# Optimization experiments

Measured on AMD Instinct MI355X. Metric: run time of the kernel, lower is better.

The kernel has to match this reference:

```python
import jax, jax.numpy as jnp
from jax import lax
import numpy as np

B, C, N, MAX_OUT = 8, 16, 2048, 100


def setup_inputs() -> dict:
    key = jax.random.key(0)
    kc, kw, ks = jax.random.split(key, 3)
    # well-formed xyxy boxes: centers in [0,1000), sizes in [1,101)
    ctr = jax.random.uniform(kc, (B, N, 2), jnp.float32) * 1000.0
    wh = jax.random.uniform(kw, (B, N, 2), jnp.float32) * 100.0 + 1.0
    boxes = jnp.concatenate([ctr - wh * 0.5, ctr + wh * 0.5], axis=-1)  # [B,N,4]
    scores = jax.random.uniform(ks, (B, C, N), jnp.float32)  # [B,C,N]
    return {
        "boxes": boxes,
        "scores": scores,
        "max_output_boxes_per_class": MAX_OUT,
        "iou_threshold": jnp.array([0.5], jnp.float32),
        "score_threshold": jnp.array([0.5], jnp.float32),
    }


def _pairwise_iou(bx):
    # bx: [N,4] xyxy -> [N,N] IoU (matches torchvision.ops.box_iou)
    x1, y1, x2, y2 = bx[:, 0], bx[:, 1], bx[:, 2], bx[:, 3]
    area = (x2 - x1) * (y2 - y1)
    iw = jnp.clip(jnp.minimum(x2[:, None], x2[None, :]) - jnp.maximum(x1[:, None], x1[None, :]), 0.0)
    ih = jnp.clip(jnp.minimum(y2[:, None], y2[None, :]) - jnp.maximum(y1[:, None], y1[None, :]), 0.0)
    inter = iw * ih
    return inter / (area[:, None] + area[None, :] - inter)


def _nms_selected(boxes, scores, iou_threshold, score_threshold, max_out):
    # boxes [B,N,4], scores [B,C,N]
    b, c, n = scores.shape
    iou = jax.vmap(_pairwise_iou)(boxes)  # [B,N,N], shared across classes
    iou_t = iou_threshold.reshape(())
    score_t = score_threshold.reshape(())

    def one_class(iou_b, cls_scores):
        order = jnp.argsort(-cls_scores)          # descending score order [N]
        valid = cls_scores[order] > score_t       # strict >, as in the torch code

        def step(suppressed, inp):
            ok, bi = inp
            kept = ok & (~suppressed[bi])
            # greedy suppression: a kept box removes all boxes with IoU > thr
            suppressed = suppressed | (kept & (iou_b[bi] > iou_t))
            return suppressed, kept

        _, keep = lax.scan(step, jnp.zeros((n,), bool), (valid, order))
        rank = jnp.cumsum(keep.astype(jnp.int32)) - 1
        sel = keep & (rank < max_out)
        pos = jnp.where(sel, rank, max_out)  # overflow/non-selected -> dropped slot
        buf = jnp.full((max_out + 1,), -1, jnp.int32).at[pos].set(
            jnp.where(sel, order.astype(jnp.int32), -1))
        return buf[:max_out]  # box indices in score order, -1 padded

    per_bc = jax.vmap(lambda iou_b, sb: jax.vmap(lambda s: one_class(iou_b, s))(sb))(iou, scores)  # [B,C,max_out]
    b_idx = jnp.broadcast_to(jnp.arange(b, dtype=jnp.int32)[:, None, None], per_bc.shape)
    c_idx = jnp.broadcast_to(jnp.arange(c, dtype=jnp.int32)[None, :, None], per_bc.shape)
    rows = jnp.stack([b_idx, c_idx, per_bc], axis=-1).reshape(-1, 3)  # [B*C*max_out, 3]
    # invalid (padded) rows are all -1
    return jnp.where(rows[:, 2:3] >= 0, rows, -1)


def reference(boxes, scores, max_output_boxes_per_class, iou_threshold, score_threshold):
    return _nms_selected(boxes, scores, iou_threshold, score_threshold,
                         int(max_output_boxes_per_class))
```

## Files before the change

kernel.cpp:

```cpp
#include <hip/hip_runtime.h>
#include <stdint.h>


#define NBOX 2048
#define THREADS 1024
#define CHUNK 128
#define MAXKEEP 256

typedef unsigned long long u64;

__device__ __forceinline__ u64 ce_x(u64 v, int s, bool up, int lane) {
  u64 p = __shfl_xor(v, s, 64);
  bool lower = ((lane & s) == 0);
  u64 mx = v > p ? v : p;
  u64 mn = v > p ? p : v;
  return (up == lower) ? mx : mn;
}

__global__ __launch_bounds__(THREADS) void nms_kernel(
    const float* __restrict__ boxes,
    const float* __restrict__ scores,
    const int* __restrict__ maxOutPtr,
    const float* __restrict__ iouThrPtr,
    const float* __restrict__ scoreThrPtr,
    int* __restrict__ out,
    int B, int C, int slots)
{
  __shared__ u64 skeys[NBOX];
  __shared__ float sx1[NBOX], sy1[NBOX], sx2[NBOX], sy2[NBOX], sar[NBOX];
  __shared__ unsigned colmask[CHUNK][4];
  __shared__ unsigned char suppPre[CHUNK];
  __shared__ int keptPos[MAXKEEP];
  __shared__ int Vsh, cntSh;

  const int tid  = threadIdx.x;
  const int lane = tid & 63;
  const int w    = tid >> 6;
  const int bc = blockIdx.x;
  const int b = bc / C, c = bc % C;
  const float iouT   = iouThrPtr[0];
  const float scoreT = scoreThrPtr[0];
  int mOut = maxOutPtr[0];
  if (mOut > slots) mOut = slots;
  if (mOut > MAXKEEP) mOut = MAXKEEP;
  if (mOut < 0) mOut = 0;

  const float* cls = scores + ((size_t)b * C + c) * NBOX;
  if (tid == 0) { Vsh = 0; cntSh = 0; }

  const int j0 = w * 128 + lane;
  const int j1 = j0 + 64;
  float s0 = cls[j0], s1 = cls[j1];
  unsigned u0 = __float_as_uint(s0); u0 = (u0 & 0x80000000u) ? ~u0 : (u0 | 0x80000000u);
  unsigned u1 = __float_as_uint(s1); u1 = (u1 & 0x80000000u) ? ~u1 : (u1 | 0x80000000u);
  u64 e0 = ((u64)u0 << 32) | (0xFFFFFFFFu - (unsigned)j0);
  u64 e1 = ((u64)u1 << 32) | (0xFFFFFFFFu - (unsigned)j1);
  int pop = __popcll(__ballot(s0 > scoreT)) + __popcll(__ballot(s1 > scoreT));

  #pragma unroll
  for (int k = 2; k <= 64; k <<= 1) {
    #pragma unroll
    for (int s = k >> 1; s >= 1; s >>= 1) {
      bool up0 = ((lane & k) == 0);
      bool up1 = (((64 + lane) & k) == 0);
      e0 = ce_x(e0, s, up0, lane);
      e1 = ce_x(e1, s, up1, lane);
    }
  }
  {
    bool up = ((w & 1) == 0);
    u64 mx = e0 > e1 ? e0 : e1, mn = e0 > e1 ? e1 : e0;
    e0 = up ? mx : mn; e1 = up ? mn : mx;
    #pragma unroll
    for (int s = 32; s >= 1; s >>= 1) {
      e0 = ce_x(e0, s, up, lane);
      e1 = ce_x(e1, s, up, lane);
    }
  }
  skeys[j0] = e0; skeys[j1] = e1;
  __syncthreads();
  if (lane == 0) atomicAdd(&Vsh, pop);

  for (int k = 256; k <= NBOX; k <<= 1) {
    for (int s = k >> 1; s >= 128; s >>= 1) {
      unsigned i = ((tid & ~(s - 1)) << 1) | (tid & (s - 1));
      unsigned jj = i | (unsigned)s;
      u64 a = skeys[i], bb = skeys[jj];
      bool up = ((i & (unsigned)k) == 0);
      bool sw = up ? (a < bb) : (a > bb);
      if (sw) { skeys[i] = bb; skeys[jj] = a; }
      __syncthreads();
    }
    e0 = skeys[j0]; e1 = skeys[j1];
    bool up = (((unsigned)(w * 128) & (unsigned)k) == 0);
    u64 mx = e0 > e1 ? e0 : e1, mn = e0 > e1 ? e1 : e0;
    e0 = up ? mx : mn; e1 = up ? mn : mx;
    #pragma unroll
    for (int s = 32; s >= 1; s >>= 1) {
      e0 = ce_x(e0, s, up, lane);
      e1 = ce_x(e1, s, up, lane);
    }
    skeys[j0] = e0; skeys[j1] = e1;
    __syncthreads();
  }

  const int V = Vsh;

  const float4* bx = (const float4*)boxes + (size_t)b * NBOX;
  for (int p = tid; p < V; p += THREADS) {
    int idx = (int)(0xFFFFFFFFu - (unsigned)skeys[p]);
    float4 f = bx[idx];
    sx1[p] = f.x; sy1[p] = f.y; sx2[p] = f.z; sy2[p] = f.w;
    sar[p] = (f.z - f.x) * (f.w - f.y);
  }
  __syncthreads();

  int cnt = 0;
  for (int c0 = 0; c0 < V && cnt < mOut; c0 += CHUNK) {
    int clen = V - c0; if (clen > CHUNK) clen = CHUNK;

    if (tid < CHUNK * 4) ((unsigned*)colmask)[tid] = 0;
    if (tid < CHUNK) suppPre[tid] = 0;
    __syncthreads();

    {
      int qo = tid & (CHUNK - 1);
      int ko = tid >> 7;
      if (qo < clen) {
        int q = c0 + qo;
        float qx1 = sx1[q], qy1 = sy1[q], qx2 = sx2[q], qy2 = sy2[q], qa = sar[q];
        int hit = 0;
        for (int k = ko; k < cnt; k += 8) {
          int kp = keptPos[k];
          float iw = fminf(sx2[kp], qx2) - fmaxf(sx1[kp], qx1);
          float ih = fminf(sy2[kp], qy2) - fmaxf(sy1[kp], qy1);
          iw = fmaxf(iw, 0.0f); ih = fmaxf(ih, 0.0f);
          float inter = iw * ih;
          float iou = inter / (sar[kp] + qa - inter);
          if (iou > iouT) hit = 1;
        }
        if (hit) suppPre[qo] = 1;
      }
    }

    {
      int i = tid & (CHUNK - 1);
      if (i < clen) {
        int ip = c0 + i;
        float ix1 = sx1[ip], iy1 = sy1[ip], ix2 = sx2[ip], iy2 = sy2[ip], ia = sar[ip];
        for (int j = tid >> 7; j < clen; j += 8) {
          if (j <= i) continue;
          int q = c0 + j;
          float iw = fminf(ix2, sx2[q]) - fmaxf(ix1, sx1[q]);
          float ih = fminf(iy2, sy2[q]) - fmaxf(iy1, sy1[q]);
          iw = fmaxf(iw, 0.0f); ih = fmaxf(ih, 0.0f);
          float inter = iw * ih;
          float iou = inter / (ia + sar[q] - inter);
          if (iou > iouT) atomicOr(&colmask[j][i >> 5], 1u << (i & 31));
        }
      }
    }
    __syncthreads();

    if (w == 0) {
      unsigned a0 = colmask[lane][0], a1 = colmask[lane][1];
      unsigned a2 = colmask[lane][2], a3 = colmask[lane][3];
      unsigned b0 = colmask[lane + 64][0], b1 = colmask[lane + 64][1];
      unsigned b2 = colmask[lane + 64][2], b3 = colmask[lane + 64][3];
      int supA = suppPre[lane];
      int supB = suppPre[lane + 64];
      int cl = cnt;
      for (int r = 0; r < clen && cl < mOut; ++r) {
        int v = (r < 64) ? supA : supB;
        int isSup = __shfl(v, r & 63);
        if (!isSup) {
          if (lane == 0) keptPos[cl] = c0 + r;
          cl++;
          unsigned wd = r >> 5, bit = r & 31;
          unsigned av = (wd == 0) ? a0 : (wd == 1) ? a1 : (wd == 2) ? a2 : a3;
          unsigned bv = (wd == 0) ? b0 : (wd == 1) ? b1 : (wd == 2) ? b2 : b3;
          supA |= (av >> bit) & 1;
          supB |= (bv >> bit) & 1;
        }
      }
      if (lane == 0) cntSh = cl;
    }
    __syncthreads();
    cnt = cntSh;
  }

  int base = bc * slots * 3;
  for (int s = tid; s < slots; s += THREADS) {
    int v = -1;
    if (s < cnt) {
      int p = keptPos[s];
      v = (int)(0xFFFFFFFFu - (unsigned)skeys[p]);
    }
    out[base + s * 3 + 0] = (v >= 0) ? b : -1;
    out[base + s * 3 + 1] = (v >= 0) ? c : -1;
    out[base + s * 3 + 2] = v;
  }
}

extern "C" void kernel_launch(void* const* d_in, const int* in_sizes, int n_in,
                              void* d_out, int out_size, void* d_ws, size_t ws_size,
                              hipStream_t stream) {
  const float* boxes  = (const float*)d_in[0];
  const float* scores = (const float*)d_in[1];
  const int*   maxOut = (const int*)d_in[2];
  const float* iouT   = (const float*)d_in[3];
  const float* scoreT = (const float*)d_in[4];
  int* out = (int*)d_out;

  const int N = NBOX;
  int B = in_sizes[0] / (4 * N);
  int C = in_sizes[1] / (B * N);
  int slots = out_size / (B * C * 3);

  nms_kernel<<<dim3(B * C), dim3(THREADS), 0, stream>>>(
      boxes, scores, maxOut, iouT, scoreT, out, B, C, slots);
}
```

Before: 92.85 us.

## Split score sort into two half-sort blocks plus final merge, ballot-based greedy scan

```diff
diff --git a/kernel.cpp b/kernel.cpp
--- a/kernel.cpp
+++ b/kernel.cpp
@@ -3,11 +3,18 @@
 
 
 #define NBOX 2048
-#define THREADS 1024
+#define HALF 1024
+#define TA 512
+#define TB 1024
 #define CHUNK 128
 #define MAXKEEP 256
 
 typedef unsigned long long u64;
+
+__device__ __forceinline__ unsigned flipf(float s) {
+  unsigned b = __float_as_uint(s);
+  return (b & 0x80000000u) ? ~b : (b | 0x80000000u);
+}
 
 __device__ __forceinline__ u64 ce_x(u64 v, int s, bool up, int lane) {
   u64 p = __shfl_xor(v, s, 64);
@@ -17,98 +24,131 @@
   return (up == lower) ? mx : mn;
 }
 
-__global__ __launch_bounds__(THREADS) void nms_kernel(
+__global__ __launch_bounds__(TA) void sort_half_kernel(
+    const float* __restrict__ scores, u64* __restrict__ wsKeys, int C)
+{
+  __shared__ u64 sk[HALF];
+  const int tid = threadIdx.x, lane = tid & 63, w = tid >> 6;
+  const int bc = blockIdx.x >> 1;
+  const int h  = blockIdx.x & 1;
+  const float* cls = scores + (size_t)bc * NBOX + h * HALF;
+
+  const int p0 = w * 128 + lane;
+  const int p1 = p0 + 64;
+  const int g0 = h * HALF + p0, g1 = h * HALF + p1;
+  u64 e0 = ((u64)flipf(cls[p0]) << 32) | (0xFFFFFFFFu - (unsigned)g0);
+  u64 e1 = ((u64)flipf(cls[p1]) << 32) | (0xFFFFFFFFu - (unsigned)g1);
+
+  #pragma unroll
+  for (int k = 2; k <= 64; k <<= 1) {
+    #pragma unroll
+    for (int s = k >> 1; s >= 1; s >>= 1) {
+      bool up0 = ((lane & k) == 0);
+      bool up1 = (((64 + lane) & k) == 0);
+      e0 = ce_x(e0, s, up0, lane);
+      e1 = ce_x(e1, s, up1, lane);
+    }
+  }
+  {
+    bool up = ((w & 1) == 0);
+    u64 mx = e0 > e1 ? e0 : e1, mn = e0 > e1 ? e1 : e0;
+    e0 = up ? mx : mn; e1 = up ? mn : mx;
+    #pragma unroll
+    for (int s = 32; s >= 1; s >>= 1) {
+      e0 = ce_x(e0, s, up, lane);
+      e1 = ce_x(e1, s, up, lane);
+    }
+  }
+  sk[p0] = e0; sk[p1] = e1;
+  __syncthreads();
+
+  for (int k = 256; k <= HALF; k <<= 1) {
+    for (int s = k >> 1; s >= 128; s >>= 1) {
+      unsigned i = ((tid & ~(s - 1)) << 1) | (tid & (s - 1));
+      unsigned j = i | (unsigned)s;
+      u64 a = sk[i], bb = sk[j];
+      bool up = ((i & (unsigned)k) == 0);
+      bool sw = up ? (a < bb) : (a > bb);
+      if (sw) { sk[i] = bb; sk[j] = a; }
+      __syncthreads();
+    }
+    e0 = sk[p0]; e1 = sk[p1];
+    bool up = (((unsigned)p0 & (unsigned)k) == 0);
+    u64 mx = e0 > e1 ? e0 : e1, mn = e0 > e1 ? e1 : e0;
+    e0 = up ? mx : mn; e1 = up ? mn : mx;
+    #pragma unroll
+    for (int s = 32; s >= 1; s >>= 1) {
+      e0 = ce_x(e0, s, up, lane);
+      e1 = ce_x(e1, s, up, lane);
+    }
+    if (k < HALF) { sk[p0] = e0; sk[p1] = e1; __syncthreads(); }
+  }
+
+  u64* dst = wsKeys + (size_t)bc * NBOX + h * HALF;
+  if (h == 0) { dst[p0] = e0; dst[p1] = e1; }
+  else        { dst[HALF - 1 - p0] = e0; dst[HALF - 1 - p1] = e1; }
+}
+
+__global__ __launch_bounds__(TB) void nms_kernel(
     const float* __restrict__ boxes,
-    const float* __restrict__ scores,
+    const u64* __restrict__ wsKeys,
     const int* __restrict__ maxOutPtr,
     const float* __restrict__ iouThrPtr,
     const float* __restrict__ scoreThrPtr,
-    int* __restrict__ out,
-    int B, int C, int slots)
+    int* __restrict__ out, int B, int C, int slots)
 {
-  __shared__ u64 skeys[NBOX];
+  __shared__ u64 sk[NBOX];
   __shared__ float sx1[NBOX], sy1[NBOX], sx2[NBOX], sy2[NBOX], sar[NBOX];
   __shared__ unsigned colmask[CHUNK][4];
   __shared__ unsigned char suppPre[CHUNK];
   __shared__ int keptPos[MAXKEEP];
   __shared__ int Vsh, cntSh;
 
-  const int tid  = threadIdx.x;
-  const int lane = tid & 63;
-  const int w    = tid >> 6;
+  const int tid = threadIdx.x, lane = tid & 63, w = tid >> 6;
   const int bc = blockIdx.x;
   const int b = bc / C, c = bc % C;
-  const float iouT   = iouThrPtr[0];
-  const float scoreT = scoreThrPtr[0];
+  const float iouT = iouThrPtr[0];
+  const unsigned thrU = flipf(scoreThrPtr[0]);
   int mOut = maxOutPtr[0];
   if (mOut > slots) mOut = slots;
   if (mOut > MAXKEEP) mOut = MAXKEEP;
   if (mOut < 0) mOut = 0;
 
-  const float* cls = scores + ((size_t)b * C + c) * NBOX;
   if (tid == 0) { Vsh = 0; cntSh = 0; }
 
-  const int j0 = w * 128 + lane;
-  const int j1 = j0 + 64;
-  float s0 = cls[j0], s1 = cls[j1];
-  unsigned u0 = __float_as_uint(s0); u0 = (u0 & 0x80000000u) ? ~u0 : (u0 | 0x80000000u);
-  unsigned u1 = __float_as_uint(s1); u1 = (u1 & 0x80000000u) ? ~u1 : (u1 | 0x80000000u);
-  u64 e0 = ((u64)u0 << 32) | (0xFFFFFFFFu - (unsigned)j0);
-  u64 e1 = ((u64)u1 << 32) | (0xFFFFFFFFu - (unsigned)j1);
-  int pop = __popcll(__ballot(s0 > scoreT)) + __popcll(__ballot(s1 > scoreT));
-
-  #pragma unroll
-  for (int k = 2; k <= 64; k <<= 1) {
-    #pragma unroll
-    for (int s = k >> 1; s >= 1; s >>= 1) {
-      bool up0 = ((lane & k) == 0);
-      bool up1 = (((64 + lane) & k) == 0);
-      e0 = ce_x(e0, s, up0, lane);
-      e1 = ce_x(e1, s, up1, lane);
-    }
+  const u64* src = wsKeys + (size_t)bc * NBOX;
+  u64 v0 = src[tid], v1 = src[tid + HALF];
+  sk[tid] = v0; sk[tid + HALF] = v1;
+  int pop = __popcll(__ballot((unsigned)(v0 >> 32) > thrU)) +
+            __popcll(__ballot((unsigned)(v1 >> 32) > thrU));
+  __syncthreads();
+  if (lane == 0) atomicAdd(&Vsh, pop);
+
+  for (int s = 1024; s >= 128; s >>= 1) {
+    unsigned i = ((tid & ~(s - 1)) << 1) | (tid & (s - 1));
+    unsigned j = i | (unsigned)s;
+    u64 a = sk[i], bb = sk[j];
+    if (a < bb) { sk[i] = bb; sk[j] = a; }
+    __syncthreads();
   }
   {
-    bool up = ((w & 1) == 0);
+    const int j0 = w * 128 + lane, j1 = j0 + 64;
+    u64 e0 = sk[j0], e1 = sk[j1];
     u64 mx = e0 > e1 ? e0 : e1, mn = e0 > e1 ? e1 : e0;
-    e0 = up ? mx : mn; e1 = up ? mn : mx;
+    e0 = mx; e1 = mn;
     #pragma unroll
     for (int s = 32; s >= 1; s >>= 1) {
-      e0 = ce_x(e0, s, up, lane);
-      e1 = ce_x(e1, s, up, lane);
-    }
-  }
-  skeys[j0] = e0; skeys[j1] = e1;
-  __syncthreads();
-  if (lane == 0) atomicAdd(&Vsh, pop);
-
-  for (int k = 256; k <= NBOX; k <<= 1) {
-    for (int s = k >> 1; s >= 128; s >>= 1) {
-      unsigned i = ((tid & ~(s - 1)) << 1) | (tid & (s - 1));
-      unsigned jj = i | (unsigned)s;
-      u64 a = skeys[i], bb = skeys[jj];
-      bool up = ((i & (unsigned)k) == 0);
-      bool sw = up ? (a < bb) : (a > bb);
-      if (sw) { skeys[i] = bb; skeys[jj] = a; }
-      __syncthreads();
-    }
-    e0 = skeys[j0]; e1 = skeys[j1];
-    bool up = (((unsigned)(w * 128) & (unsigned)k) == 0);
-    u64 mx = e0 > e1 ? e0 : e1, mn = e0 > e1 ? e1 : e0;
-    e0 = up ? mx : mn; e1 = up ? mn : mx;
-    #pragma unroll
-    for (int s = 32; s >= 1; s >>= 1) {
-      e0 = ce_x(e0, s, up, lane);
-      e1 = ce_x(e1, s, up, lane);
-    }
-    skeys[j0] = e0; skeys[j1] = e1;
-    __syncthreads();
-  }
-
+      e0 = ce_x(e0, s, true, lane);
+      e1 = ce_x(e1, s, true, lane);
+    }
+    sk[j0] = e0; sk[j1] = e1;
+  }
+  __syncthreads();
   const int V = Vsh;
 
   const float4* bx = (const float4*)boxes + (size_t)b * NBOX;
-  for (int p = tid; p < V; p += THREADS) {
-    int idx = (int)(0xFFFFFFFFu - (unsigned)skeys[p]);
+  for (int p = tid; p < V; p += TB) {
+    int idx = (int)(0xFFFFFFFFu - (unsigned)sk[p]);
     float4 f = bx[idx];
     sx1[p] = f.x; sy1[p] = f.y; sx2[p] = f.z; sy2[p] = f.w;
     sar[p] = (f.z - f.x) * (f.w - f.y);
@@ -164,24 +204,36 @@
 
     if (w == 0) {
       unsigned a0 = colmask[lane][0], a1 = colmask[lane][1];
-      unsigned a2 = colmask[lane][2], a3 = colmask[lane][3];
       unsigned b0 = colmask[lane + 64][0], b1 = colmask[lane + 64][1];
       unsigned b2 = colmask[lane + 64][2], b3 = colmask[lane + 64][3];
-      int supA = suppPre[lane];
-      int supB = suppPre[lane + 64];
+      bool supA = (lane < clen) ? (suppPre[lane] != 0) : true;
+      bool supB = (lane + 64 < clen) ? (suppPre[lane + 64] != 0) : true;
+      bool doneA = (lane >= clen);
+      bool doneB = (lane + 64 >= clen);
       int cl = cnt;
-      for (int r = 0; r < clen && cl < mOut; ++r) {
-        int v = (r < 64) ? supA : supB;
-        int isSup = __shfl(v, r & 63);
-        if (!isSup) {
-          if (lane == 0) keptPos[cl] = c0 + r;
-          cl++;
-          unsigned wd = r >> 5, bit = r & 31;
-          unsigned av = (wd == 0) ? a0 : (wd == 1) ? a1 : (wd == 2) ? a2 : a3;
-          unsigned bv = (wd == 0) ? b0 : (wd == 1) ? b1 : (wd == 2) ? b2 : b3;
-          supA |= (av >> bit) & 1;
-          supB |= (bv >> bit) & 1;
-        }
+      while (cl < mOut) {
+        u64 cand = __ballot(!doneA && !supA);
+        if (!cand) break;
+        int r = __ffsll((long long)cand) - 1;
+        if (lane == 0) keptPos[cl] = c0 + r;
+        cl++;
+        if (lane == r) doneA = true;
+        unsigned av = (r < 32) ? a0 : a1;
+        unsigned bv = (r < 32) ? b0 : b1;
+        unsigned bit = (unsigned)r & 31;
+        supA = supA || ((av >> bit) & 1);
+        supB = supB || ((bv >> bit) & 1);
+      }
+      while (cl < mOut) {
+        u64 cand = __ballot(!doneB && !supB);
+        if (!cand) break;
+        int r = __ffsll((long long)cand) - 1;
+        if (lane == 0) keptPos[cl] = c0 + 64 + r;
+        cl++;
+        if (lane == r) doneB = true;
+        unsigned bv = (r < 32) ? b2 : b3;
+        unsigned bit = (unsigned)r & 31;
+        supB = supB || ((bv >> bit) & 1);
       }
       if (lane == 0) cntSh = cl;
     }
@@ -190,11 +242,11 @@
   }
 
   int base = bc * slots * 3;
-  for (int s = tid; s < slots; s += THREADS) {
+  for (int s = tid; s < slots; s += TB) {
     int v = -1;
     if (s < cnt) {
       int p = keptPos[s];
-      v = (int)(0xFFFFFFFFu - (unsigned)skeys[p]);
+      v = (int)(0xFFFFFFFFu - (unsigned)sk[p]);
     }
     out[base + s * 3 + 0] = (v >= 0) ? b : -1;
     out[base + s * 3 + 1] = (v >= 0) ? c : -1;
@@ -211,12 +263,14 @@
   const float* iouT   = (const float*)d_in[3];
   const float* scoreT = (const float*)d_in[4];
   int* out = (int*)d_out;
+  u64* wsKeys = (u64*)d_ws;
 
   const int N = NBOX;
   int B = in_sizes[0] / (4 * N);
   int C = in_sizes[1] / (B * N);
   int slots = out_size / (B * C * 3);
 
-  nms_kernel<<<dim3(B * C), dim3(THREADS), 0, stream>>>(
-      boxes, scores, maxOut, iouT, scoreT, out, B, C, slots);
-}
+  sort_half_kernel<<<dim3(B * C * 2), dim3(TA), 0, stream>>>(scores, wsKeys, C);
+  nms_kernel<<<dim3(B * C), dim3(TB), 0, stream>>>(
+      boxes, wsKeys, maxOut, iouT, scoreT, out, B, C, slots);
+}
```

Measured after the change: 89.57 us. 3.5% less time.
